# Optimization experiments

Measured on AMD Instinct MI355X. Metric: run time of the kernel, lower is better.

The kernel has to match this reference:

```python
import jax, jax.numpy as jnp
import numpy as np

B, N, D, H = 4, 2048, 1024, 16
HD = D // H
SCALE = HD ** -0.5

def neg_softmax(x):
    # sign(x) * softmax(|x|) along last axis
    return jnp.sign(x) * jax.nn.softmax(jnp.abs(x), axis=-1)

def setup_inputs() -> dict:
    key = jax.random.key(0)
    ks = jax.random.split(key, 9)
    s = 0.02
    return {
        "x": jax.random.normal(ks[0], (B, N, D), jnp.float32),
        "Wq": jax.random.normal(ks[1], (D, D), jnp.float32) * s,
        "bq": jax.random.normal(ks[2], (D,), jnp.float32) * s,
        "Wk": jax.random.normal(ks[3], (D, D), jnp.float32) * s,
        "bk": jax.random.normal(ks[4], (D,), jnp.float32) * s,
        "Wv": jax.random.normal(ks[5], (D, D), jnp.float32) * s,
        "bv": jax.random.normal(ks[6], (D,), jnp.float32) * s,
        "Wo": jax.random.normal(ks[7], (D, D), jnp.float32) * s,
        "bo": jax.random.normal(ks[8], (D,), jnp.float32) * s,
    }

def reference(x, Wq, bq, Wk, bk, Wv, bv, Wo, bo):
    def heads(t):  # [B,N,D] -> [B,H,N,hd]
        return t.reshape(B, N, H, HD).transpose(0, 2, 1, 3)
    Q = heads(x @ Wq.T + bq)
    K = heads(x @ Wk.T + bk)
    V = heads(x @ Wv.T + bv)
    logits = jnp.einsum('bhnd,bhmd->bhnm', Q, K) * SCALE
    attn = neg_softmax(logits)
    out = jnp.einsum('bhnm,bhmd->bhnd', attn, V)
    out = out.transpose(0, 2, 1, 3).reshape(B, N, D)
    return out @ Wo.T + bo
```

## Files before the change

kernel.cpp:

```cpp
#include <hip/hip_runtime.h>

typedef _Float16 f16x8 __attribute__((ext_vector_type(8)));
typedef __fp16 h16x2 __attribute__((ext_vector_type(2)));
typedef float f32x4 __attribute__((ext_vector_type(4)));
typedef unsigned short u16x4 __attribute__((ext_vector_type(4)));

#define NB 4
#define NSEQ 2048
#define NH 16
#define HDIM 64
#define DM 1024
#define MROWS (NB * NSEQ)

__device__ __forceinline__ float exp2_fast(float x) {
  float r; asm("v_exp_f32 %0, %1" : "=v"(r) : "v"(x)); return r;
}

__device__ __forceinline__ unsigned short f2h(float f) {
  _Float16 h = (_Float16)f;
  union { _Float16 h; unsigned short u; } v; v.h = h;
  return v.u;
}

__global__ void cvt_kernel(const float* __restrict__ in, unsigned short* __restrict__ out, int n4) {
  int i = blockIdx.x * blockDim.x + threadIdx.x;
  if (i < n4) {
    const float4 v = ((const float4*)in)[i];
    u16x4 o;
    o.x = f2h(v.x); o.y = f2h(v.y); o.z = f2h(v.z); o.w = f2h(v.w);
    ((u16x4*)out)[i] = o;
  }
}

template<int OUT_F16>
__global__ __launch_bounds__(256)
void gemm_bt(const unsigned short* __restrict__ A, const unsigned short* __restrict__ Bw,
             const float* __restrict__ bias, void* __restrict__ Cv, float scale) {
  __shared__ unsigned short As[128 * 32];
  __shared__ unsigned short Bs[128 * 32];
  const int tid = threadIdx.x, lane = tid & 63, wave = tid >> 6;
  const int g = lane >> 4, c = lane & 15;
  const int orig = blockIdx.y * 8 + blockIdx.x;
  const int wg = (orig & 7) * 64 + (orig >> 3);
  const int m0 = (wg >> 3) * 128, n0 = (wg & 7) * 128;
  const int wm = (wave >> 1) * 64, wn = (wave & 1) * 64;
  f32x4 acc[4][4] = {};
  for (int kt = 0; kt < 1024; kt += 32) {
#pragma unroll
    for (int p = 0; p < 2; ++p) {
      const int idx = p * 256 + tid;
      const int row = idx >> 2, col = (idx & 3) * 8;
      __builtin_amdgcn_global_load_lds(
          (const __attribute__((address_space(1))) void*)(A + (size_t)(m0 + row) * 1024 + kt + col),
          (__attribute__((address_space(3))) void*)(As + idx * 8), 16, 0, 0);
      __builtin_amdgcn_global_load_lds(
          (const __attribute__((address_space(1))) void*)(Bw + (size_t)(n0 + row) * 1024 + kt + col),
          (__attribute__((address_space(3))) void*)(Bs + idx * 8), 16, 0, 0);
    }
    __syncthreads();
    f16x8 af[4], bfr[4];
#pragma unroll
    for (int i = 0; i < 4; ++i) af[i] = *(const f16x8*)(As + (wm + i * 16 + c) * 32 + g * 8);
#pragma unroll
    for (int i = 0; i < 4; ++i) bfr[i] = *(const f16x8*)(Bs + (wn + i * 16 + c) * 32 + g * 8);
#pragma unroll
    for (int i = 0; i < 4; ++i)
#pragma unroll
      for (int j = 0; j < 4; ++j)
        acc[i][j] = __builtin_amdgcn_mfma_f32_16x16x32_f16(af[i], bfr[j], acc[i][j], 0, 0, 0);
    __syncthreads();
  }
#pragma unroll
  for (int i = 0; i < 4; ++i)
#pragma unroll
    for (int j = 0; j < 4; ++j)
#pragma unroll
      for (int r = 0; r < 4; ++r) {
        const int row = m0 + wm + i * 16 + g * 4 + r;
        const int col = n0 + wn + j * 16 + c;
        const float v = (acc[i][j][r] + bias[col]) * scale;
        if (OUT_F16) ((unsigned short*)Cv)[(size_t)row * 1024 + col] = f2h(v);
        else         ((float*)Cv)[(size_t)row * 1024 + col] = v;
      }
}

__global__ __launch_bounds__(256)
void attn_kernel(const unsigned short* __restrict__ Qg, const unsigned short* __restrict__ Kg,
                 const unsigned short* __restrict__ Vg, unsigned short* __restrict__ Og) {
  __shared__ __align__(16) unsigned short Kl[2][64 * 64];
  __shared__ __align__(16) unsigned short Vt[2][64 * 72];
  const int tid = threadIdx.x, lane = tid & 63, wave = tid >> 6;
  const int g = lane >> 4, c = lane & 15;
  const int b = blockIdx.y >> 4, h = blockIdx.y & 15;
  const int q0 = blockIdx.x * 128 + wave * 32;
  const size_t rb = (size_t)b * NSEQ;
  const int hc = h * HDIM;
  const int NT = NSEQ / 64;

  const int k_kvo = tid >> 3;
  const int k_d   = (((tid & 7) ^ ((tid >> 3) & 7)) * 8);
  const int v_kv = lane;
  const int pv = (v_kv & 32) | (((v_kv >> 2) & 3) << 3) | (((v_kv >> 4) & 1) << 2) | (v_kv & 3);

  f16x8 qf[2][2];
#pragma unroll
  for (int m = 0; m < 2; ++m)
#pragma unroll
    for (int kb2 = 0; kb2 < 2; ++kb2)
      qf[m][kb2] = *(const f16x8*)(Qg + (rb + q0 + m * 16 + c) * DM + hc + kb2 * 32 + g * 8);

  f32x4 oT[4][2] = {};
  float dpart[2] = {0.f, 0.f};
  f16x8 vreg[2];

  auto stageK = [&](int t, int buf) {
    const int kv0 = t * 64;
#pragma unroll
    for (int p = 0; p < 2; ++p) {
      const int kv = kv0 + 32 * p + k_kvo;
      __builtin_amdgcn_global_load_lds(
          (const __attribute__((address_space(1))) void*)(Kg + (rb + kv) * DM + hc + k_d),
          (__attribute__((address_space(3))) void*)(&Kl[buf][p * 2048 + tid * 8]), 16, 0, 0);
    }
  };
  auto loadV = [&](int t) {
    const int kv0 = t * 64;
#pragma unroll
    for (int p = 0; p < 2; ++p)
      vreg[p] = *(const f16x8*)(Vg + (rb + kv0 + v_kv) * DM + hc + p * 32 + wave * 8);
  };
  auto writeV = [&](int buf) {
#pragma unroll
    for (int p = 0; p < 2; ++p) {
      const int vd = p * 32 + wave * 8;
      union { f16x8 v; unsigned short u[8]; } vv; vv.v = vreg[p];
#pragma unroll
      for (int j = 0; j < 8; ++j) Vt[buf][(vd + j) * 72 + pv] = vv.u[j];
    }
  };

  stageK(0, 0);
  loadV(0);
  writeV(0);
  __syncthreads();

  for (int t = 0; t < NT; ++t) {
    const int cur = t & 1;
    if (t + 1 < NT) { stageK(t + 1, cur ^ 1); loadV(t + 1); }

    const unsigned short* KL = Kl[cur];
    const unsigned short* VT = Vt[cur];

    f16x8 kf[2][4];
#pragma unroll
    for (int kb2 = 0; kb2 < 2; ++kb2)
#pragma unroll
      for (int nb = 0; nb < 4; ++nb)
        kf[kb2][nb] = *(const f16x8*)(KL + (nb * 16 + c) * 64 + (((kb2 * 32 + g * 8) ^ ((c & 7) * 8))));
    f32x4 s[2][4] = {};
#pragma unroll
    for (int m = 0; m < 2; ++m)
#pragma unroll
      for (int nb = 0; nb < 4; ++nb)
#pragma unroll
        for (int kb2 = 0; kb2 < 2; ++kb2)
          s[m][nb] = __builtin_amdgcn_mfma_f32_16x16x32_f16(kf[kb2][nb], qf[m][kb2], s[m][nb], 0, 0, 0);

    f16x8 vtf[2][4];
#pragma unroll
    for (int kb2 = 0; kb2 < 2; ++kb2)
#pragma unroll
      for (int db = 0; db < 4; ++db)
        vtf[kb2][db] = *(const f16x8*)(VT + (db * 16 + c) * 72 + kb2 * 32 + g * 8);

#pragma unroll
    for (int m = 0; m < 2; ++m) {
      union PW { f16x8 v; h16x2 w[4]; } pf[2];
#pragma unroll
      for (int nb = 0; nb < 4; ++nb) {
        float p[4];
#pragma unroll
        for (int r = 0; r < 4; ++r) {
          const float sv = s[m][nb][r];
          const float e = exp2_fast(fabsf(sv) - 18.0f);
          dpart[m] += e;
          p[r] = copysignf(e, sv);
        }
        pf[nb >> 1].w[(nb & 1) * 2]     = __builtin_amdgcn_cvt_pkrtz(p[0], p[1]);
        pf[nb >> 1].w[(nb & 1) * 2 + 1] = __builtin_amdgcn_cvt_pkrtz(p[2], p[3]);
      }
#pragma unroll
      for (int db = 0; db < 4; ++db) {
        oT[db][m] = __builtin_amdgcn_mfma_f32_16x16x32_f16(vtf[0][db], pf[0].v, oT[db][m], 0, 0, 0);
        oT[db][m] = __builtin_amdgcn_mfma_f32_16x16x32_f16(vtf[1][db], pf[1].v, oT[db][m], 0, 0, 0);
      }
    }

    if (t + 1 < NT) writeV(cur ^ 1);
    __syncthreads();
  }

#pragma unroll
  for (int m = 0; m < 2; ++m) {
    float d = dpart[m];
    d += __shfl_xor(d, 16);
    d += __shfl_xor(d, 32);
    const float inv = 1.f / d;
#pragma unroll
    for (int db = 0; db < 4; ++db) {
      h16x2 h01 = __builtin_amdgcn_cvt_pkrtz(oT[db][m][0] * inv, oT[db][m][1] * inv);
      h16x2 h23 = __builtin_amdgcn_cvt_pkrtz(oT[db][m][2] * inv, oT[db][m][3] * inv);
      union { h16x2 h; unsigned u; } a, bb; a.h = h01; bb.h = h23;
      union { uint2 u2; unsigned u[2]; } st;
      st.u[0] = a.u; st.u[1] = bb.u;
      *(uint2*)(Og + (rb + q0 + m * 16 + c) * DM + hc + db * 16 + g * 4) = st.u2;
    }
  }
}

extern "C" void kernel_launch(void* const* d_in, const int* in_sizes, int n_in,
                              void* d_out, int out_size, void* d_ws, size_t ws_size,
                              hipStream_t stream) {
  const float* x  = (const float*)d_in[0];
  const float* Wq = (const float*)d_in[1];
  const float* bq = (const float*)d_in[2];
  const float* Wk = (const float*)d_in[3];
  const float* bk = (const float*)d_in[4];
  const float* Wv = (const float*)d_in[5];
  const float* bv = (const float*)d_in[6];
  const float* Wo = (const float*)d_in[7];
  const float* bo = (const float*)d_in[8];
  float* out = (float*)d_out;

  unsigned short* xb  = (unsigned short*)d_ws;
  unsigned short* wqb = xb  + (size_t)MROWS * DM;
  unsigned short* wkb = wqb + (size_t)DM * DM;
  unsigned short* wvb = wkb + (size_t)DM * DM;
  unsigned short* wob = wvb + (size_t)DM * DM;
  unsigned short* qb  = wob + (size_t)DM * DM;
  unsigned short* kb  = qb  + (size_t)MROWS * DM;
  unsigned short* vb  = kb  + (size_t)MROWS * DM;
  unsigned short* ab  = xb;

  cvt_kernel<<<(MROWS * DM) / 1024, 256, 0, stream>>>(x,  xb,  (MROWS * DM) / 4);
  cvt_kernel<<<(DM * DM) / 1024,   256, 0, stream>>>(Wq, wqb, (DM * DM) / 4);
  cvt_kernel<<<(DM * DM) / 1024,   256, 0, stream>>>(Wk, wkb, (DM * DM) / 4);
  cvt_kernel<<<(DM * DM) / 1024,   256, 0, stream>>>(Wv, wvb, (DM * DM) / 4);
  cvt_kernel<<<(DM * DM) / 1024,   256, 0, stream>>>(Wo, wob, (DM * DM) / 4);

  const dim3 gg(DM / 128, MROWS / 128);
  const float SC = 0.125f * 1.4426950408889634f;
  gemm_bt<1><<<gg, 256, 0, stream>>>(xb, wqb, bq, qb, SC);
  gemm_bt<1><<<gg, 256, 0, stream>>>(xb, wkb, bk, kb, 1.f);
  gemm_bt<1><<<gg, 256, 0, stream>>>(xb, wvb, bv, vb, 1.f);

  attn_kernel<<<dim3(NSEQ / 128, NB * NH), 256, 0, stream>>>(qb, kb, vb, ab);

  gemm_bt<0><<<gg, 256, 0, stream>>>(ab, wob, bo, out, 1.f);
}
```

Baseline: 234.6 us.

## Merge weight conversions, remap attention blocks, add occupancy hint, batch denominator sums

Replaces four separate weight-conversion launches with one 2D-grid kernel that picks the source and destination by blockIdx.y, removing launch overhead. Remaps the attention grid so consecutive workgroups are spread across heads and batches, likely to improve cache locality or XCD balance. Adds a min-blocks-per-CU hint of 3 to the attention kernel, which may force register spills. Accumulates the softmax denominator into a local sum before adding it to the running total, shortening the dependency chain.

Result: faster. 225.3 us (-4.0%).

```diff
diff --git a/kernel.cpp b/kernel.cpp
--- a/kernel.cpp
+++ b/kernel.cpp
@@ -11,6 +11,9 @@
 #define HDIM 64
 #define DM 1024
 #define MROWS (NB * NSEQ)
+
+#define AS1 __attribute__((address_space(1)))
+#define AS3 __attribute__((address_space(3)))
 
 __device__ __forceinline__ float exp2_fast(float x) {
   float r; asm("v_exp_f32 %0, %1" : "=v"(r) : "v"(x)); return r;
@@ -30,6 +33,24 @@
     o.x = f2h(v.x); o.y = f2h(v.y); o.z = f2h(v.z); o.w = f2h(v.w);
     ((u16x4*)out)[i] = o;
   }
+}
+
+__global__ void cvt4_kernel(const float* __restrict__ w0, const float* __restrict__ w1,
+                            const float* __restrict__ w2, const float* __restrict__ w3,
+                            unsigned short* __restrict__ o0, unsigned short* __restrict__ o1,
+                            unsigned short* __restrict__ o2, unsigned short* __restrict__ o3) {
+  const int i = blockIdx.x * blockDim.x + threadIdx.x;
+  const float* src; unsigned short* dst;
+  switch (blockIdx.y) {
+    case 0: src = w0; dst = o0; break;
+    case 1: src = w1; dst = o1; break;
+    case 2: src = w2; dst = o2; break;
+    default: src = w3; dst = o3; break;
+  }
+  const float4 v = ((const float4*)src)[i];
+  u16x4 o;
+  o.x = f2h(v.x); o.y = f2h(v.y); o.z = f2h(v.z); o.w = f2h(v.w);
+  ((u16x4*)dst)[i] = o;
 }
 
 template<int OUT_F16>
@@ -51,11 +72,11 @@
       const int idx = p * 256 + tid;
       const int row = idx >> 2, col = (idx & 3) * 8;
       __builtin_amdgcn_global_load_lds(
-          (const __attribute__((address_space(1))) void*)(A + (size_t)(m0 + row) * 1024 + kt + col),
-          (__attribute__((address_space(3))) void*)(As + idx * 8), 16, 0, 0);
+          (const AS1 void*)(A + (size_t)(m0 + row) * 1024 + kt + col),
+          (AS3 void*)(As + idx * 8), 16, 0, 0);
       __builtin_amdgcn_global_load_lds(
-          (const __attribute__((address_space(1))) void*)(Bw + (size_t)(n0 + row) * 1024 + kt + col),
-          (__attribute__((address_space(3))) void*)(Bs + idx * 8), 16, 0, 0);
+          (const AS1 void*)(Bw + (size_t)(n0 + row) * 1024 + kt + col),
+          (AS3 void*)(Bs + idx * 8), 16, 0, 0);
     }
     __syncthreads();
     f16x8 af[4], bfr[4];
@@ -84,15 +105,18 @@
       }
 }
 
-__global__ __launch_bounds__(256)
+__global__ __launch_bounds__(256, 3)
 void attn_kernel(const unsigned short* __restrict__ Qg, const unsigned short* __restrict__ Kg,
                  const unsigned short* __restrict__ Vg, unsigned short* __restrict__ Og) {
   __shared__ __align__(16) unsigned short Kl[2][64 * 64];
   __shared__ __align__(16) unsigned short Vt[2][64 * 72];
   const int tid = threadIdx.x, lane = tid & 63, wave = tid >> 6;
   const int g = lane >> 4, c = lane & 15;
-  const int b = blockIdx.y >> 4, h = blockIdx.y & 15;
-  const int q0 = blockIdx.x * 128 + wave * 32;
+  const int orig = blockIdx.y * 16 + blockIdx.x;
+  const int wg = (orig & 7) * 128 + (orig >> 3);
+  const int qblk = wg & 15, bh = wg >> 4;
+  const int b = bh >> 4, h = bh & 15;
+  const int q0 = qblk * 128 + wave * 32;
   const size_t rb = (size_t)b * NSEQ;
   const int hc = h * HDIM;
   const int NT = NSEQ / 64;
@@ -119,8 +143,8 @@
     for (int p = 0; p < 2; ++p) {
       const int kv = kv0 + 32 * p + k_kvo;
       __builtin_amdgcn_global_load_lds(
-          (const __attribute__((address_space(1))) void*)(Kg + (rb + kv) * DM + hc + k_d),
-          (__attribute__((address_space(3))) void*)(&Kl[buf][p * 2048 + tid * 8]), 16, 0, 0);
+          (const AS1 void*)(Kg + (rb + kv) * DM + hc + k_d),
+          (AS3 void*)(&Kl[buf][p * 2048 + tid * 8]), 16, 0, 0);
     }
   };
   auto loadV = [&](int t) {
@@ -176,6 +200,7 @@
 #pragma unroll
     for (int m = 0; m < 2; ++m) {
       union PW { f16x8 v; h16x2 w[4]; } pf[2];
+      float es = 0.f;
 #pragma unroll
       for (int nb = 0; nb < 4; ++nb) {
         float p[4];
@@ -183,12 +208,13 @@
         for (int r = 0; r < 4; ++r) {
           const float sv = s[m][nb][r];
           const float e = exp2_fast(fabsf(sv) - 18.0f);
-          dpart[m] += e;
+          es += e;
           p[r] = copysignf(e, sv);
         }
         pf[nb >> 1].w[(nb & 1) * 2]     = __builtin_amdgcn_cvt_pkrtz(p[0], p[1]);
         pf[nb >> 1].w[(nb & 1) * 2 + 1] = __builtin_amdgcn_cvt_pkrtz(p[2], p[3]);
       }
+      dpart[m] += es;
 #pragma unroll
       for (int db = 0; db < 4; ++db) {
         oT[db][m] = __builtin_amdgcn_mfma_f32_16x16x32_f16(vtf[0][db], pf[0].v, oT[db][m], 0, 0, 0);
@@ -242,11 +268,8 @@
   unsigned short* vb  = kb  + (size_t)MROWS * DM;
   unsigned short* ab  = xb;
 
-  cvt_kernel<<<(MROWS * DM) / 1024, 256, 0, stream>>>(x,  xb,  (MROWS * DM) / 4);
-  cvt_kernel<<<(DM * DM) / 1024,   256, 0, stream>>>(Wq, wqb, (DM * DM) / 4);
-  cvt_kernel<<<(DM * DM) / 1024,   256, 0, stream>>>(Wk, wkb, (DM * DM) / 4);
-  cvt_kernel<<<(DM * DM) / 1024,   256, 0, stream>>>(Wv, wvb, (DM * DM) / 4);
-  cvt_kernel<<<(DM * DM) / 1024,   256, 0, stream>>>(Wo, wob, (DM * DM) / 4);
+  cvt_kernel<<<(MROWS * DM) / 1024, 256, 0, stream>>>(x, xb, (MROWS * DM) / 4);
+  cvt4_kernel<<<dim3((DM * DM) / 1024, 4), 256, 0, stream>>>(Wq, Wk, Wv, Wo, wqb, wkb, wvb, wob);
 
   const dim3 gg(DM / 128, MROWS / 128);
   const float SC = 0.125f * 1.4426950408889634f;
```
